# Optimization experiments

Hardware: AMD Instinct MI355X
Metric: run time of the kernel (lower is better)

## Reference

```python
import jax, jax.numpy as jnp
import numpy as np

H, W = 4096, 4096

# Fixed tiny kernels expressed as shifted-slice sums (exactly equivalent to
# F.conv2d with stride=1, padding=0 for these 0/1 kernels).

def _diag(x):   # [[1,0],[0,1]] -> (H-1, W-1)
    return x[:-1, :-1] + x[1:, 1:]

def _anti(x):   # [[0,1],[1,0]]
    return x[:-1, 1:] + x[1:, :-1]

def _all2(x):   # 2x2 all-ones
    return x[:-1, :-1] + x[:-1, 1:] + x[1:, :-1] + x[1:, 1:]

def _cross(x):  # 3x3 plus-shape -> (H-2, W-2)
    return x[:-2, 1:-1] + x[2:, 1:-1] + x[1:-1, :-2] + x[1:-1, 2:]

def setup_inputs() -> dict:
    key = jax.random.key(0)
    board = jax.random.randint(key, (H, W), 0, 3, dtype=jnp.int32)
    return {"board_np": board}

def reference(board_np):
    black = (board_np == 1).astype(jnp.float32)
    white = (board_np == 2).astype(jnp.float32)
    empty = (board_np == 0).astype(jnp.float32)

    black_diag, black_anti = _diag(black), _anti(black)
    white_diag, white_anti = _diag(white), _anti(white)
    empty_diag, empty_anti = _diag(empty), _anti(empty)

    bamboo_black = ((black_diag == 2) & (empty_anti == 2)) | ((black_anti == 2) & (empty_diag == 2))
    bamboo_white = ((white_diag == 2) & (empty_anti == 2)) | ((white_anti == 2) & (empty_diag == 2))

    black_s2, white_s2, empty_s2 = _all2(black), _all2(white), _all2(empty)
    # tmp_de/ae/be/ce: single-cell picks of the 2x2 window
    empty_d = empty[1:, 1:]
    empty_a = empty[:-1, :-1]
    empty_b = empty[:-1, 1:]
    empty_c = empty[1:, :-1]
    any_empty_corner = (empty_d == 1) | (empty_a == 1) | (empty_b == 1) | (empty_c == 1)

    tiger_black = (black_s2 >= 2) & any_empty_corner
    tiger_white = (white_s2 >= 2) & any_empty_corner
    empty_triangle_black = (black_s2 == 3) & (empty_s2 == 1)
    empty_triangle_white = (white_s2 == 3) & (empty_s2 == 1)

    empty_center = empty[1:-1, 1:-1]  # k_center conv
    eye_black = (empty_center == 1) & (_cross(black) == 4)
    eye_white = (empty_center == 1) & (_cross(white) == 4)

    return (bamboo_black, bamboo_white, tiger_black, tiger_white,
            empty_triangle_black, empty_triangle_white, eye_black, eye_white)
```

## Files before the change

### kernel.cpp

```cpp
#include <hip/hip_runtime.h>
#include <cstdint>


#define BW 4096
#define W1 4095
#define W2 4094
#define N1 16769025
#define N2 16760836
#define M55 0x5555u

typedef int i4a __attribute__((vector_size(16), aligned(16)));

struct Planes { unsigned pm[6]; unsigned em[2]; };

__device__ __forceinline__ Planes compute_swar(unsigned m0, unsigned m1, unsigned m2)
{
    const unsigned B0 = m0 & M55,        W0 = (m0 >> 1) & M55;
    const unsigned B1 = m1 & M55,        Wl = (m1 >> 1) & M55;
    const unsigned B2 = m2 & M55,        W2m = (m2 >> 1) & M55;
    const unsigned E0 = (B0 | W0) ^ M55;
    const unsigned E1 = (B1 | Wl) ^ M55;

    const unsigned sB0 = B0 >> 2, sB1 = B1 >> 2;
    const unsigned sW0 = W0 >> 2, sW1 = Wl >> 2;
    const unsigned sE0 = E0 >> 2, sE1 = E1 >> 2;
    const unsigned sB2 = B2 >> 2, sW2 = W2m >> 2;

    const unsigned EaEd = E0 & sE1;
    const unsigned EbEc = sE0 & E1;
    const unsigned anyE = E0 | sE0 | E1 | sE1;

    Planes r;
    {
        const unsigned P = B0 & sB0, Q = B1 & sB1;
        const unsigned Dg = B0 & sB1, Ag = sB0 & B1;
        const unsigned X = B0 & B1,  Y = sB0 & sB1;
        const unsigned ge2 = P | Q | Dg | Ag | X | Y;
        const unsigned ge3 = (P & (B1 | sB1)) | (Q & (B0 | sB0));
        r.pm[0] = (Dg & EbEc) | (Ag & EaEd);
        r.pm[2] = ge2 & anyE;
        r.pm[4] = ge3 & anyE;
        r.em[0] = sE1 & sB0 & B1 & (B1 >> 4) & sB2;
    }
    {
        const unsigned P = W0 & sW0, Q = Wl & sW1;
        const unsigned Dg = W0 & sW1, Ag = sW0 & Wl;
        const unsigned X = W0 & Wl,  Y = sW0 & sW1;
        const unsigned ge2 = P | Q | Dg | Ag | X | Y;
        const unsigned ge3 = (P & (Wl | sW1)) | (Q & (W0 | sW0));
        r.pm[1] = (Dg & EbEc) | (Ag & EaEd);
        r.pm[3] = ge2 & anyE;
        r.pm[5] = ge3 & anyE;
        r.em[1] = sE1 & sW0 & Wl & (Wl >> 4) & sW2;
    }
    return r;
}

template<int PH>
__device__ __forceinline__ void store_row(
    int* __restrict__ out, const int i, const int u, const bool has2,
    const Planes& pl)
{
    const bool fullv = (u < 1023);
    const size_t orow = (size_t)i * W1 + (u << 2);

    #pragma unroll
    for (int p = 0; p < 6; ++p) {
        const int sp = (PH - p) & 3;
        int* dst = out + (size_t)p * N1 + orow;
        if (fullv) {
            i4a s;
            s[0] = (int)((pl.pm[p] >> (2 * (sp + 0))) & 1);
            s[1] = (int)((pl.pm[p] >> (2 * (sp + 1))) & 1);
            s[2] = (int)((pl.pm[p] >> (2 * (sp + 2))) & 1);
            s[3] = (int)((pl.pm[p] >> (2 * (sp + 3))) & 1);
            *(i4a*)(dst + sp) = s;
        } else {
            #pragma unroll
            for (int k = 0; k < 3 - sp; ++k)
                dst[sp + k] = (int)((pl.pm[p] >> (2 * (sp + k))) & 1);
        }
        if (u == 0) {
            #pragma unroll
            for (int k = 0; k < sp; ++k)
                dst[k] = (int)((pl.pm[p] >> (2 * k)) & 1);
        }
    }

    if (has2) {
        const int e = (PH & 1) ? 0 : 2;
        int* d0 = out + (size_t)6 * N1 + (size_t)i * W2 + (u << 2);
        int* d1 = d0 + N2;
        if (fullv) {
            i4a s0, s1;
            #pragma unroll
            for (int k = 0; k < 4; ++k) {
                s0[k] = (int)((pl.em[0] >> (2 * (e + k))) & 1);
                s1[k] = (int)((pl.em[1] >> (2 * (e + k))) & 1);
            }
            *(i4a*)(d0 + e) = s0;
            *(i4a*)(d1 + e) = s1;
        } else if (e == 0) {
            #pragma unroll
            for (int k = 0; k < 2; ++k) {
                d0[k] = (int)((pl.em[0] >> (2 * k)) & 1);
                d1[k] = (int)((pl.em[1] >> (2 * k)) & 1);
            }
        }
        if (u == 0) {
            #pragma unroll
            for (int k = 0; k < e; ++k) {
                d0[k] = (int)((pl.em[0] >> (2 * k)) & 1);
                d1[k] = (int)((pl.em[1] >> (2 * k)) & 1);
            }
        }
    }
}

template<int I0M4>
__device__ __forceinline__ void strip_body(
    const int* __restrict__ board, int* __restrict__ out,
    const int u, const int i0)
{
    const int base = u << 2;
    const bool fullv = (u < 1023);
    const bool lastStrip = (i0 == W1 - 1);

    const int rC = (i0 + 2 <= W1) ? i0 + 2 : W1;
    const int rD = (i0 + 3 <= W1) ? i0 + 3 : W1;

    const int* pA = board + (size_t)i0 * BW + base;
    const int* pB = board + (size_t)(i0 + 1) * BW + base;
    const int* pC = board + (size_t)rC * BW + base;
    const int* pD = board + (size_t)rD * BW + base;
    i4a vA = *(const i4a*)pA;
    i4a vB = *(const i4a*)pB;
    i4a vC = *(const i4a*)pC;
    i4a vD = *(const i4a*)pD;
    i4a xA = {0,0,0,0}, xB = {0,0,0,0}, xC = {0,0,0,0}, xD = {0,0,0,0};
    if (fullv) {
        xA = *(const i4a*)(pA + 4);
        xB = *(const i4a*)(pB + 4);
        xC = *(const i4a*)(pC + 4);
        xD = *(const i4a*)(pD + 4);
    }

    auto pack = [](const i4a& v, const i4a& x) -> unsigned {
        return (unsigned)(v[0] | (v[1] << 2) | (v[2] << 4) | (v[3] << 6)
                        | (x[0] << 8) | (x[1] << 10) | (x[2] << 12) | (x[3] << 14));
    };
    const unsigned m0 = pack(vA, xA);
    const unsigned m1 = pack(vB, xB);
    const unsigned m2 = pack(vC, xC);
    const unsigned m3 = pack(vD, xD);

    Planes P0 = compute_swar(m0, m1, m2);
    store_row<I0M4>(out, i0, u, !lastStrip, P0);

    if (!lastStrip) {
        Planes P1 = compute_swar(m1, m2, m3);
        store_row<(I0M4 + 1) & 3>(out, i0 + 1, u, true, P1);
    }
}

__global__ __launch_bounds__(256)
void motif_kernel(const int* __restrict__ board, int* __restrict__ out) {
    const int u  = blockIdx.x * 256 + threadIdx.x;
    const int i0 = blockIdx.y << 1;

    if ((i0 & 2) == 0) strip_body<0>(board, out, u, i0);
    else               strip_body<2>(board, out, u, i0);
}

extern "C" void kernel_launch(void* const* d_in, const int* in_sizes, int n_in,
                              void* d_out, int out_size, void* d_ws, size_t ws_size,
                              hipStream_t stream) {
    const int* board = (const int*)d_in[0];
    int* out = (int*)d_out;

    dim3 block(256, 1, 1);
    dim3 grid(4, 2048, 1);
    motif_kernel<<<grid, block, 0, stream>>>(board, out);
}
```

Before: 584.3 us.

## Process four output rows per thread and use nontemporal stores

Each thread now loads six board rows and produces four output rows instead of four rows for two, which cuts redundant input reads. The grid is halved to match. Output vector stores become nontemporal to stream the large write-only outputs past the cache. The cost is more registers per thread and fewer threads in flight.

```diff
diff --git a/kernel.cpp b/kernel.cpp
--- a/kernel.cpp
+++ b/kernel.cpp
@@ -74,7 +74,7 @@
             s[1] = (int)((pl.pm[p] >> (2 * (sp + 1))) & 1);
             s[2] = (int)((pl.pm[p] >> (2 * (sp + 2))) & 1);
             s[3] = (int)((pl.pm[p] >> (2 * (sp + 3))) & 1);
-            *(i4a*)(dst + sp) = s;
+            __builtin_nontemporal_store(s, (i4a*)(dst + sp));
         } else {
             #pragma unroll
             for (int k = 0; k < 3 - sp; ++k)
@@ -98,8 +98,8 @@
                 s0[k] = (int)((pl.em[0] >> (2 * (e + k))) & 1);
                 s1[k] = (int)((pl.em[1] >> (2 * (e + k))) & 1);
             }
-            *(i4a*)(d0 + e) = s0;
-            *(i4a*)(d1 + e) = s1;
+            __builtin_nontemporal_store(s0, (i4a*)(d0 + e));
+            __builtin_nontemporal_store(s1, (i4a*)(d1 + e));
         } else if (e == 0) {
             #pragma unroll
             for (int k = 0; k < 2; ++k) {
@@ -117,59 +117,54 @@
     }
 }
 
-template<int I0M4>
-__device__ __forceinline__ void strip_body(
-    const int* __restrict__ board, int* __restrict__ out,
-    const int u, const int i0)
-{
-    const int base = u << 2;
-    const bool fullv = (u < 1023);
-    const bool lastStrip = (i0 == W1 - 1);
-
-    const int rC = (i0 + 2 <= W1) ? i0 + 2 : W1;
-    const int rD = (i0 + 3 <= W1) ? i0 + 3 : W1;
-
-    const int* pA = board + (size_t)i0 * BW + base;
-    const int* pB = board + (size_t)(i0 + 1) * BW + base;
-    const int* pC = board + (size_t)rC * BW + base;
-    const int* pD = board + (size_t)rD * BW + base;
-    i4a vA = *(const i4a*)pA;
-    i4a vB = *(const i4a*)pB;
-    i4a vC = *(const i4a*)pC;
-    i4a vD = *(const i4a*)pD;
-    i4a xA = {0,0,0,0}, xB = {0,0,0,0}, xC = {0,0,0,0}, xD = {0,0,0,0};
-    if (fullv) {
-        xA = *(const i4a*)(pA + 4);
-        xB = *(const i4a*)(pB + 4);
-        xC = *(const i4a*)(pC + 4);
-        xD = *(const i4a*)(pD + 4);
-    }
-
-    auto pack = [](const i4a& v, const i4a& x) -> unsigned {
-        return (unsigned)(v[0] | (v[1] << 2) | (v[2] << 4) | (v[3] << 6)
-                        | (x[0] << 8) | (x[1] << 10) | (x[2] << 12) | (x[3] << 14));
-    };
-    const unsigned m0 = pack(vA, xA);
-    const unsigned m1 = pack(vB, xB);
-    const unsigned m2 = pack(vC, xC);
-    const unsigned m3 = pack(vD, xD);
-
-    Planes P0 = compute_swar(m0, m1, m2);
-    store_row<I0M4>(out, i0, u, !lastStrip, P0);
-
-    if (!lastStrip) {
-        Planes P1 = compute_swar(m1, m2, m3);
-        store_row<(I0M4 + 1) & 3>(out, i0 + 1, u, true, P1);
-    }
-}
-
 __global__ __launch_bounds__(256)
 void motif_kernel(const int* __restrict__ board, int* __restrict__ out) {
     const int u  = blockIdx.x * 256 + threadIdx.x;
-    const int i0 = blockIdx.y << 1;
+    const int i0 = blockIdx.y << 2;
+    const int base = u << 2;
+    const bool fullv = (u < 1023);
+    const bool last = (i0 == W1 - 3);
 
-    if ((i0 & 2) == 0) strip_body<0>(board, out, u, i0);
-    else               strip_body<2>(board, out, u, i0);
+    const int* pr[6];
+    #pragma unroll
+    for (int j = 0; j < 6; ++j) {
+        int r = i0 + j; if (r > W1) r = W1;
+        pr[j] = board + (size_t)r * BW + base;
+    }
+    i4a v[6], x[6];
+    #pragma unroll
+    for (int j = 0; j < 6; ++j) v[j] = *(const i4a*)pr[j];
+    #pragma unroll
+    for (int j = 0; j < 6; ++j) x[j] = (i4a){0,0,0,0};
+    if (fullv) {
+        #pragma unroll
+        for (int j = 0; j < 6; ++j) x[j] = *(const i4a*)(pr[j] + 4);
+    }
+
+    auto pack = [](const i4a& vv, const i4a& xx) -> unsigned {
+        return (unsigned)(vv[0] | (vv[1] << 2) | (vv[2] << 4) | (vv[3] << 6)
+                        | (xx[0] << 8) | (xx[1] << 10) | (xx[2] << 12) | (xx[3] << 14));
+    };
+    unsigned m[6];
+    #pragma unroll
+    for (int j = 0; j < 6; ++j) m[j] = pack(v[j], x[j]);
+
+    {
+        Planes P = compute_swar(m[0], m[1], m[2]);
+        store_row<0>(out, i0, u, true, P);
+    }
+    {
+        Planes P = compute_swar(m[1], m[2], m[3]);
+        store_row<1>(out, i0 + 1, u, true, P);
+    }
+    {
+        Planes P = compute_swar(m[2], m[3], m[4]);
+        store_row<2>(out, i0 + 2, u, !last, P);
+    }
+    if (!last) {
+        Planes P = compute_swar(m[3], m[4], m[5]);
+        store_row<3>(out, i0 + 3, u, true, P);
+    }
 }
 
 extern "C" void kernel_launch(void* const* d_in, const int* in_sizes, int n_in,
@@ -179,6 +174,6 @@
     int* out = (int*)d_out;
 
     dim3 block(256, 1, 1);
-    dim3 grid(4, 2048, 1);
+    dim3 grid(4, 1024, 1);
     motif_kernel<<<grid, block, 0, stream>>>(board, out);
 }
```

New measurement: 613.2 us. +4.9%, slower.
